# Kernel optimization log

Hardware: AMD Instinct MI355X
Metric: run time of the kernel (lower is better)

The kernel has to match this reference:

```python
import jax, jax.numpy as jnp
import numpy as np


def setup_inputs() -> dict:
    key = jax.random.key(0)
    x = jax.random.normal(key, (16, 64, 512, 512), dtype=jnp.float32)
    return {"x": x}


def reference(x) -> jnp.ndarray:
    # PartialDerivative with dim=0: diagonal (c,c,2,1) kernel with weights
    # [-1, +1] along H == forward finite difference along the H axis.
    # out[b,c,h,w] = x[b,c,h+1,w] - x[b,c,h,w], shape (b, c, h-1, w)
    return x[:, :, 1:, :] - x[:, :, :-1, :]
```

## Files before the change

kernel.cpp:

```cpp
#include <hip/hip_runtime.h>


typedef float f32x4 __attribute__((ext_vector_type(4)));

#define H_IN   512
#define H_OUT  511
#define W4     128
#define CHUNKS 8
#define CH_H   64

__global__ __launch_bounds__(256) void PartialDerivative_kernel(
    const f32x4* __restrict__ x, f32x4* __restrict__ out) {
    const int t  = blockIdx.x * 256 + threadIdx.x;
    const int w4 = t & (W4 - 1);
    const int ck = (t >> 7) & (CHUNKS - 1);
    const int bc = t >> 10;

    const int h0   = ck * CH_H;
    const int nout = (ck == CHUNKS - 1) ? (CH_H - 1) : CH_H;

    const f32x4* xp = x   + (size_t)bc * (H_IN * W4)  + (size_t)h0 * W4 + w4;
    f32x4*       op = out + (size_t)bc * (H_OUT * W4) + (size_t)h0 * W4 + w4;

    f32x4 prev = xp[0];
    #pragma unroll 4
    for (int i = 0; i < nout; ++i) {
        f32x4 nxt = xp[(size_t)(i + 1) * W4];
        f32x4 r = nxt - prev;
        __builtin_nontemporal_store(r, &op[(size_t)i * W4]);
        prev = nxt;
    }
}

extern "C" void kernel_launch(void* const* d_in, const int* in_sizes, int n_in,
                              void* d_out, int out_size, void* d_ws, size_t ws_size,
                              hipStream_t stream) {
    const f32x4* x = (const f32x4*)d_in[0];
    f32x4* out = (f32x4*)d_out;

    dim3 block(256);
    dim3 grid((16 * 64 * CHUNKS * W4) / 256);
    PartialDerivative_kernel<<<grid, block, 0, stream>>>(x, out);
}
```

Before: 430.7 us.

## Replace per-thread H-chunk streaming with flat grid-stride elementwise difference

```diff
diff --git a/kernel.cpp b/kernel.cpp
--- a/kernel.cpp
+++ b/kernel.cpp
@@ -3,32 +3,21 @@
 
 typedef float f32x4 __attribute__((ext_vector_type(4)));
 
-#define H_IN   512
-#define H_OUT  511
-#define W4     128
-#define CHUNKS 8
-#define CH_H   64
+#define W4        128
+#define PLANE_OUT (511 * W4)
+#define TOTAL_OUT (1024u * PLANE_OUT)
+#define NBLOCKS   2048
 
 __global__ __launch_bounds__(256) void PartialDerivative_kernel(
     const f32x4* __restrict__ x, f32x4* __restrict__ out) {
-    const int t  = blockIdx.x * 256 + threadIdx.x;
-    const int w4 = t & (W4 - 1);
-    const int ck = (t >> 7) & (CHUNKS - 1);
-    const int bc = t >> 10;
-
-    const int h0   = ck * CH_H;
-    const int nout = (ck == CHUNKS - 1) ? (CH_H - 1) : CH_H;
-
-    const f32x4* xp = x   + (size_t)bc * (H_IN * W4)  + (size_t)h0 * W4 + w4;
-    f32x4*       op = out + (size_t)bc * (H_OUT * W4) + (size_t)h0 * W4 + w4;
-
-    f32x4 prev = xp[0];
-    #pragma unroll 4
-    for (int i = 0; i < nout; ++i) {
-        f32x4 nxt = xp[(size_t)(i + 1) * W4];
-        f32x4 r = nxt - prev;
-        __builtin_nontemporal_store(r, &op[(size_t)i * W4]);
-        prev = nxt;
+    const unsigned stride = NBLOCKS * 256;
+    for (unsigned idx = blockIdx.x * 256 + threadIdx.x; idx < TOTAL_OUT;
+         idx += stride) {
+        const unsigned plane = idx / PLANE_OUT;
+        const size_t in_idx = (size_t)idx + (size_t)plane * W4;
+        f32x4 a = x[in_idx];
+        f32x4 b = x[in_idx + W4];
+        out[idx] = b - a;
     }
 }
 
@@ -37,8 +26,5 @@
                               hipStream_t stream) {
     const f32x4* x = (const f32x4*)d_in[0];
     f32x4* out = (f32x4*)d_out;
-
-    dim3 block(256);
-    dim3 grid((16 * 64 * CHUNKS * W4) / 256);
-    PartialDerivative_kernel<<<grid, block, 0, stream>>>(x, out);
+    PartialDerivative_kernel<<<dim3(NBLOCKS), dim3(256), 0, stream>>>(x, out);
 }
```

After: 435.8 us. Within noise of the previous version (+1.2%).
